# Optimization experiments

Hardware: AMD Instinct MI355X
Metric: run time of the kernel (lower is better)

The kernel has to match this reference:

```python
import jax, jax.numpy as jnp
import numpy as np

D_MODEL = 512
NUM_HEADS = 8
D_HEAD = D_MODEL // NUM_HEADS
B, S = 2, 4096


def setup_inputs() -> dict:
    key = jax.random.key(0)
    ks = jax.random.split(key, 9)
    scale = 1.0 / np.sqrt(D_MODEL)
    x = jax.random.normal(ks[0], (B, S, D_MODEL), dtype=jnp.float32)
    Wq = jax.random.normal(ks[1], (D_MODEL, D_MODEL), dtype=jnp.float32) * scale
    Wk = jax.random.normal(ks[2], (D_MODEL, D_MODEL), dtype=jnp.float32) * scale
    Wv = jax.random.normal(ks[3], (D_MODEL, D_MODEL), dtype=jnp.float32) * scale
    Wo = jax.random.normal(ks[4], (D_MODEL, D_MODEL), dtype=jnp.float32) * scale
    bq = jnp.zeros((D_MODEL,), jnp.float32)
    bk = jnp.zeros((D_MODEL,), jnp.float32)
    bv = jnp.zeros((D_MODEL,), jnp.float32)
    bo = jnp.zeros((D_MODEL,), jnp.float32)
    return {"x": x, "Wq": Wq, "bq": bq, "Wk": Wk, "bk": bk,
            "Wv": Wv, "bv": bv, "Wo": Wo, "bo": bo}


def _split_heads(t):
    # [B, S, D] -> [B, H, S, d_head]
    b, s, _ = t.shape
    return t.reshape(b, s, NUM_HEADS, D_HEAD).transpose(0, 2, 1, 3)


def reference(x, Wq, bq, Wk, bk, Wv, bv, Wo, bo):
    q = _split_heads(x @ Wq + bq)  # [B,H,S,dh]
    k = _split_heads(x @ Wk + bk)
    v = _split_heads(x @ Wv + bv)
    scores = jnp.einsum("bhqd,bhkd->bhqk", q, k) / jnp.sqrt(
        jnp.asarray(D_HEAD, x.dtype))
    attn = jax.nn.softmax(scores, axis=-1)  # dropout is identity at inference
    out = jnp.einsum("bhqk,bhkd->bhqd", attn, v)  # [B,H,S,dh]
    out = out.transpose(0, 2, 1, 3).reshape(x.shape[0], x.shape[1], D_MODEL)
    return out @ Wo + bo
```

## Files before the change

kernel.cpp:

```cpp
#include <hip/hip_runtime.h>
#include <cstddef>

#define NB   2
#define SEQ  4096
#define DM   512
#define NH   8
#define DH   64
#define MTOT 8192
#define KSPLIT 2
#define KSEQ (SEQ / KSPLIT)

#define QSCALE 0.18033688011112042f

typedef __attribute__((ext_vector_type(8))) short short8;
typedef __attribute__((ext_vector_type(4))) float f32x4;

__device__ __forceinline__ ushort f2bf(float f) {
  unsigned u = __builtin_bit_cast(unsigned, f);
  u += 0x7FFFu + ((u >> 16) & 1u);
  return (ushort)(u >> 16);
}
__device__ __forceinline__ float bf2f(ushort b) {
  return __builtin_bit_cast(float, ((unsigned)b) << 16);
}
__device__ __forceinline__ unsigned cvt_pk_bf16(float lo, float hi) {
  unsigned r;
  asm("v_cvt_pk_bf16_f32 %0, %1, %2" : "=v"(r) : "v"(lo), "v"(hi));
  return r;
}
__device__ __forceinline__ float fexp2(float x) {
#if __has_builtin(__builtin_amdgcn_exp2f)
  return __builtin_amdgcn_exp2f(x);
#else
  float r;
  asm("v_exp_f32 %0, %1" : "=v"(r) : "v"(x));
  return r;
#endif
}

__global__ __launch_bounds__(256)
void xcast_k(const float* __restrict__ x, ushort* __restrict__ xb) {
  const int i = (blockIdx.x * 256 + threadIdx.x) * 8;
  float4 a = *(const float4*)(x + i);
  float4 b = *(const float4*)(x + i + 4);
  ushort h[8] = {f2bf(a.x), f2bf(a.y), f2bf(a.z), f2bf(a.w),
                 f2bf(b.x), f2bf(b.y), f2bf(b.z), f2bf(b.w)};
  *(uint4*)(xb + i) = *(const uint4*)h;
}

__global__ __launch_bounds__(256)
void prep_w_k(const float* __restrict__ W, ushort* __restrict__ WT,
              ushort* __restrict__ WTl) {
  __shared__ float t[32][33];
  const int k0 = blockIdx.x * 32, n0 = blockIdx.y * 32;
  const int tx = threadIdx.x & 31, ty = threadIdx.x >> 5;
#pragma unroll
  for (int i = 0; i < 32; i += 8)
    t[ty + i][tx] = W[(size_t)(k0 + ty + i) * DM + n0 + tx];
  __syncthreads();
#pragma unroll
  for (int i = 0; i < 32; i += 8) {
    float v = t[tx][ty + i];
    ushort h = f2bf(v);
    WT[(size_t)(n0 + ty + i) * DM + k0 + tx] = h;
    if (WTl) WTl[(size_t)(n0 + ty + i) * DM + k0 + tx] = f2bf(v - bf2f(h));
  }
}

__global__ __launch_bounds__(256)
void qkv_gemm_k(const ushort* __restrict__ xb,
                const ushort* __restrict__ WTq, const ushort* __restrict__ WTk,
                const ushort* __restrict__ WTv,
                const float* __restrict__ bq, const float* __restrict__ bk,
                const float* __restrict__ bv,
                ushort* __restrict__ Qb, ushort* __restrict__ Kb,
                ushort* __restrict__ Vb) {
  __shared__ ushort smem[64 * 136];
  ushort (*As)[40] = (ushort(*)[40])smem;
  ushort (*Bs)[40] = (ushort(*)[40])(smem + 5120);

  const int z = blockIdx.z;
  const ushort* WT = (z == 0) ? WTq : (z == 1) ? WTk : WTv;
  const float* bias = (z == 0) ? bq : (z == 1) ? bk : bv;
  ushort* outp = (z == 0) ? Qb : (z == 1) ? Kb : Vb;
  const float oscale = (z == 0) ? QSCALE : 1.0f;

  const int tid = threadIdx.x;
  const int w = tid >> 6, l = tid & 63;
  const int g = l >> 4, l15 = l & 15;
  const int wm = w >> 1, wn = w & 1;
  const int m0 = blockIdx.x * 128;
  const int n0 = blockIdx.y * 64;

  const int ar = tid >> 1, ac = (tid & 1) * 16;
  const int br = tid >> 2, bc = (tid & 3) * 8;

  const ushort* Ag = xb + (size_t)(m0 + ar) * DM + ac;
  const ushort* Bg = WT + (size_t)(n0 + br) * DM + bc;

  uint4 ra0 = *(const uint4*)(Ag);
  uint4 ra1 = *(const uint4*)(Ag + 8);
  uint4 rb0 = *(const uint4*)(Bg);

  float bfn[2];
#pragma unroll
  for (int fn = 0; fn < 2; ++fn)
    bfn[fn] = bias[n0 + wn * 32 + fn * 16 + l15];

  f32x4 acc[4][2];
#pragma unroll
  for (int fm = 0; fm < 4; ++fm)
#pragma unroll
    for (int fn = 0; fn < 2; ++fn) acc[fm][fn] = (f32x4){0.f, 0.f, 0.f, 0.f};

  for (int k0 = 0; k0 < DM; k0 += 32) {
    __syncthreads();
    *(uint4*)&As[ar][ac] = ra0;
    *(uint4*)&As[ar][ac + 8] = ra1;
    *(uint4*)&Bs[br][bc] = rb0;
    __syncthreads();
    if (k0 + 32 < DM) {
      ra0 = *(const uint4*)(Ag + k0 + 32);
      ra1 = *(const uint4*)(Ag + k0 + 40);
      rb0 = *(const uint4*)(Bg + k0 + 32);
    }
    short8 af[4], bf[2];
#pragma unroll
    for (int fm = 0; fm < 4; ++fm)
      af[fm] = *(const short8*)&As[wm * 64 + fm * 16 + l15][g * 8];
#pragma unroll
    for (int fn = 0; fn < 2; ++fn)
      bf[fn] = *(const short8*)&Bs[wn * 32 + fn * 16 + l15][g * 8];
#pragma unroll
    for (int fm = 0; fm < 4; ++fm)
#pragma unroll
      for (int fn = 0; fn < 2; ++fn)
        acc[fm][fn] = __builtin_amdgcn_mfma_f32_16x16x32_bf16(
            af[fm], bf[fn], acc[fm][fn], 0, 0, 0);
  }

  if (z != 2) {
#pragma unroll
    for (int fm = 0; fm < 4; ++fm)
#pragma unroll
      for (int fn = 0; fn < 2; ++fn)
#pragma unroll
        for (int r = 0; r < 4; ++r) {
          int m = m0 + wm * 64 + fm * 16 + g * 4 + r;
          int n = n0 + wn * 32 + fn * 16 + l15;
          float v = (acc[fm][fn][r] + bfn[fn]) * oscale;
          int b = m >> 12, s = m & (SEQ - 1);
          int h = n >> 6, d = n & 63;
          outp[(size_t)((b * NH + h) * SEQ + s) * DH + d] = f2bf(v);
        }
  } else {
    __syncthreads();
    ushort (*T)[136] = (ushort(*)[136])smem;
#pragma unroll
    for (int fm = 0; fm < 4; ++fm)
#pragma unroll
      for (int fn = 0; fn < 2; ++fn)
#pragma unroll
        for (int r = 0; r < 4; ++r) {
          int ml = wm * 64 + fm * 16 + g * 4 + r;
          int nl = wn * 32 + fn * 16 + l15;
          T[nl][ml] = f2bf(acc[fm][fn][r] + bfn[fn]);
        }
    __syncthreads();
    const int b = m0 >> 12, h = n0 >> 6, s0 = m0 & (SEQ - 1);
#pragma unroll
    for (int it = 0; it < 4; ++it) {
      int ch = tid + 256 * it;
      int row = ch >> 4;
      int cc = (ch & 15) * 8;
      *(uint4*)&outp[((size_t)(b * NH + h) * DH + row) * SEQ + s0 + cc] =
          *(const uint4*)&T[row][cc];
    }
  }
}

__global__ __launch_bounds__(256)
void oproj_gemm_k(const float* __restrict__ Po, const float* __restrict__ Dn,
                  const ushort* __restrict__ WTh, const ushort* __restrict__ WTl,
                  const float* __restrict__ bo, float* __restrict__ out) {
  __shared__ ushort Ah[128][40];
  __shared__ ushort Al[128][40];
  __shared__ ushort Bh[64][40];
  __shared__ ushort Bl[64][40];

  const int tid = threadIdx.x;
  const int w = tid >> 6, l = tid & 63;
  const int g = l >> 4, l15 = l & 15;
  const int wm = w >> 1, wn = w & 1;
  const int m0 = blockIdx.x * 128;
  const int n0 = blockIdx.y * 64;

  const int ar = tid >> 1, ac = (tid & 1) * 16;
  const int br = tid >> 2, bc = (tid & 3) * 8;

  const int m  = m0 + ar;
  const int bb = m >> 12, ss = m & (SEQ - 1);
  const size_t zoff = (size_t)(NB * NH) * SEQ * DH;

  const ushort* Bhg = WTh + (size_t)(n0 + br) * DM + bc;
  const ushort* Blg = WTl + (size_t)(n0 + br) * DM + bc;

  auto loadA = [&](int c, float* av) {
    const int h = c >> 6, d = c & 63;
    const int bh = bb * NH + h;
    const size_t i0 = ((size_t)bh * SEQ + ss) * DH + d;
    const float den = Dn[(size_t)bh * SEQ + ss] +
                      Dn[(size_t)(NB * NH + bh) * SEQ + ss];
    const float inv = __builtin_amdgcn_rcpf(den);
#pragma unroll
    for (int i = 0; i < 16; i += 4) {
      float4 p0 = *(const float4*)(Po + i0 + i);
      float4 p1 = *(const float4*)(Po + zoff + i0 + i);
      av[i + 0] = (p0.x + p1.x) * inv;
      av[i + 1] = (p0.y + p1.y) * inv;
      av[i + 2] = (p0.z + p1.z) * inv;
      av[i + 3] = (p0.w + p1.w) * inv;
    }
  };

  float av[16];
  loadA(ac, av);
  uint4 rbh = *(const uint4*)Bhg;
  uint4 rbl = *(const uint4*)Blg;

  float bfn[2];
#pragma unroll
  for (int fn = 0; fn < 2; ++fn)
    bfn[fn] = bo[n0 + wn * 32 + fn * 16 + l15];

  f32x4 acc[4][2];
#pragma unroll
  for (int fm = 0; fm < 4; ++fm)
#pragma unroll
    for (int fn = 0; fn < 2; ++fn) acc[fm][fn] = (f32x4){0.f, 0.f, 0.f, 0.f};

  for (int k0 = 0; k0 < DM; k0 += 32) {
    __syncthreads();
    {
      ushort hh[16], ll[16];
#pragma unroll
      for (int i = 0; i < 16; ++i) {
        ushort h = f2bf(av[i]);
        hh[i] = h;
        ll[i] = f2bf(av[i] - bf2f(h));
      }
      *(uint4*)&Ah[ar][ac]     = *(const uint4*)&hh[0];
      *(uint4*)&Ah[ar][ac + 8] = *(const uint4*)&hh[8];
      *(uint4*)&Al[ar][ac]     = *(const uint4*)&ll[0];
      *(uint4*)&Al[ar][ac + 8] = *(const uint4*)&ll[8];
      *(uint4*)&Bh[br][bc] = rbh;
      *(uint4*)&Bl[br][bc] = rbl;
    }
    __syncthreads();
    if (k0 + 32 < DM) {
      loadA(ac + k0 + 32, av);
      rbh = *(const uint4*)(Bhg + k0 + 32);
      rbl = *(const uint4*)(Blg + k0 + 32);
    }
    short8 ah[4], al[4], bh[2], bl[2];
#pragma unroll
    for (int fm = 0; fm < 4; ++fm) {
      ah[fm] = *(const short8*)&Ah[wm * 64 + fm * 16 + l15][g * 8];
      al[fm] = *(const short8*)&Al[wm * 64 + fm * 16 + l15][g * 8];
    }
#pragma unroll
    for (int fn = 0; fn < 2; ++fn) {
      bh[fn] = *(const short8*)&Bh[wn * 32 + fn * 16 + l15][g * 8];
      bl[fn] = *(const short8*)&Bl[wn * 32 + fn * 16 + l15][g * 8];
    }
#pragma unroll
    for (int fm = 0; fm < 4; ++fm)
#pragma unroll
      for (int fn = 0; fn < 2; ++fn) {
        f32x4 c = acc[fm][fn];
        c = __builtin_amdgcn_mfma_f32_16x16x32_bf16(ah[fm], bh[fn], c, 0, 0, 0);
        c = __builtin_amdgcn_mfma_f32_16x16x32_bf16(ah[fm], bl[fn], c, 0, 0, 0);
        c = __builtin_amdgcn_mfma_f32_16x16x32_bf16(al[fm], bh[fn], c, 0, 0, 0);
        acc[fm][fn] = c;
      }
  }

#pragma unroll
  for (int fm = 0; fm < 4; ++fm)
#pragma unroll
    for (int fn = 0; fn < 2; ++fn)
#pragma unroll
      for (int r = 0; r < 4; ++r) {
        int mm = m0 + wm * 64 + fm * 16 + g * 4 + r;
        int n = n0 + wn * 32 + fn * 16 + l15;
        out[(size_t)mm * DM + n] = acc[fm][fn][r] + bfn[fn];
      }
}

__global__ __launch_bounds__(256, 4)
void attn_mfma_k(const ushort* __restrict__ Q, const ushort* __restrict__ K,
                 const ushort* __restrict__ VT, float* __restrict__ Po,
                 float* __restrict__ Dn) {
  __shared__ ushort Ks[2][64][72];
  __shared__ unsigned Vt[2][64][36];

  const int tid = threadIdx.x;
  const int w   = tid >> 6;
  const int l   = tid & 63;
  const int g   = l >> 4;
  const int l15 = l & 15;
  const int bh  = blockIdx.y;
  const int z   = blockIdx.z;
  const int q0  = blockIdx.x * 128 + w * 32;
  const int tb  = z * KSEQ;

  short8 qb[2][2];
#pragma unroll
  for (int qh = 0; qh < 2; ++qh) {
    const ushort* Qrow = Q + ((size_t)bh * SEQ + q0 + qh * 16 + l15) * DH;
    qb[qh][0] = *(const short8*)(Qrow + g * 8);
    qb[qh][1] = *(const short8*)(Qrow + 32 + g * 8);
  }

  short8 vones;
#pragma unroll
  for (int i = 0; i < 8; ++i) vones[i] = (short)0x3F80;

  f32x4 acc[2][4];
  f32x4 accl[2];
#pragma unroll
  for (int qh = 0; qh < 2; ++qh) {
    accl[qh] = (f32x4){0.f, 0.f, 0.f, 0.f};
#pragma unroll
    for (int dt = 0; dt < 4; ++dt) acc[qh][dt] = (f32x4){0.f, 0.f, 0.f, 0.f};
  }

  const ushort* Kg = K + (size_t)bh * SEQ * DH;

  const int rho  = tid >> 2;
  const int kcol = (tid & 3) * 16;
  const int sig  = 32 * ((rho >> 5) & 1) + 8 * ((rho >> 2) & 3) +
                   4 * ((rho >> 4) & 1) + (rho & 3);
  const ushort* Kp = Kg + (size_t)(tb + sig) * DH + kcol;

  const int vrow = tid >> 2;
  const int vcb  = (tid & 3) * 8;
  const unsigned* Vrow =
      (const unsigned*)(VT + ((size_t)bh * DH + vrow) * SEQ) + tb / 2 + vcb;

  uint4 kr0 = *(const uint4*)(Kp);
  uint4 kr1 = *(const uint4*)(Kp + 8);
  uint4 vv0 = *(const uint4*)(Vrow);
  uint4 vv1 = *(const uint4*)(Vrow + 4);

  int cur = 0;
  for (int t0 = 0; t0 < KSEQ; t0 += 64) {
    *(uint4*)&Ks[cur][rho][kcol]     = kr0;
    *(uint4*)&Ks[cur][rho][kcol + 8] = kr1;
    *(uint4*)&Vt[cur][vrow][vcb]     = vv0;
    *(uint4*)&Vt[cur][vrow][vcb + 4] = vv1;
    if (t0 + 64 < KSEQ) {
      kr0 = *(const uint4*)(Kp + (size_t)(t0 + 64) * DH);
      kr1 = *(const uint4*)(Kp + (size_t)(t0 + 64) * DH + 8);
      vv0 = *(const uint4*)(Vrow + (t0 + 64) / 2);
      vv1 = *(const uint4*)(Vrow + (t0 + 64) / 2 + 4);
    }
    __syncthreads();

    f32x4 s[2][4];
    __builtin_amdgcn_s_setprio(1);
#pragma unroll
    for (int nf = 0; nf < 4; ++nf) {
      short8 ka0 = *(const short8*)&Ks[cur][nf * 16 + l15][g * 8];
      short8 ka1 = *(const short8*)&Ks[cur][nf * 16 + l15][32 + g * 8];
#pragma unroll
      for (int qh = 0; qh < 2; ++qh) {
        f32x4 c = (f32x4){0.f, 0.f, 0.f, 0.f};
        c = __builtin_amdgcn_mfma_f32_16x16x32_bf16(ka0, qb[qh][0], c, 0, 0, 0);
        c = __builtin_amdgcn_mfma_f32_16x16x32_bf16(ka1, qb[qh][1], c, 0, 0, 0);
        s[qh][nf] = c;
      }
    }
    __builtin_amdgcn_s_setprio(0);

    short8 pa[2][2];
#pragma unroll
    for (int qh = 0; qh < 2; ++qh) {
      float p[4][4];
#pragma unroll
      for (int nf = 0; nf < 4; ++nf)
#pragma unroll
        for (int r = 0; r < 4; ++r) p[nf][r] = fexp2(s[qh][nf][r]);
      uint4 u0, u1;
      u0.x = cvt_pk_bf16(p[0][0], p[0][1]);
      u0.y = cvt_pk_bf16(p[0][2], p[0][3]);
      u0.z = cvt_pk_bf16(p[1][0], p[1][1]);
      u0.w = cvt_pk_bf16(p[1][2], p[1][3]);
      u1.x = cvt_pk_bf16(p[2][0], p[2][1]);
      u1.y = cvt_pk_bf16(p[2][2], p[2][3]);
      u1.z = cvt_pk_bf16(p[3][0], p[3][1]);
      u1.w = cvt_pk_bf16(p[3][2], p[3][3]);
      pa[qh][0] = __builtin_bit_cast(short8, u0);
      pa[qh][1] = __builtin_bit_cast(short8, u1);
    }

    __builtin_amdgcn_s_setprio(1);
#pragma unroll
    for (int dt = 0; dt < 4; ++dt) {
      short8 vb0 = *(const short8*)&Vt[cur][dt * 16 + l15][4 * g];
      short8 vb1 = *(const short8*)&Vt[cur][dt * 16 + l15][16 + 4 * g];
#pragma unroll
      for (int qh = 0; qh < 2; ++qh) {
        acc[qh][dt] = __builtin_amdgcn_mfma_f32_16x16x32_bf16(pa[qh][0], vb0,
                                                              acc[qh][dt], 0, 0, 0);
        acc[qh][dt] = __builtin_amdgcn_mfma_f32_16x16x32_bf16(pa[qh][1], vb1,
                                                              acc[qh][dt], 0, 0, 0);
      }
    }
#pragma unroll
    for (int qh = 0; qh < 2; ++qh) {
      accl[qh] = __builtin_amdgcn_mfma_f32_16x16x32_bf16(pa[qh][0], vones,
                                                         accl[qh], 0, 0, 0);
      accl[qh] = __builtin_amdgcn_mfma_f32_16x16x32_bf16(pa[qh][1], vones,
                                                         accl[qh], 0, 0, 0);
    }
    __builtin_amdgcn_s_setprio(0);
    cur ^= 1;
  }

  const int zo = z * (NB * NH) + bh;
#pragma unroll
  for (int qh = 0; qh < 2; ++qh) {
#pragma unroll
    for (int dt = 0; dt < 4; ++dt)
#pragma unroll
      for (int r = 0; r < 4; ++r) {
        int srow = q0 + qh * 16 + g * 4 + r;
        Po[((size_t)zo * SEQ + srow) * DH + dt * 16 + l15] = acc[qh][dt][r];
      }
    if (l15 == 0)
#pragma unroll
      for (int r = 0; r < 4; ++r)
        Dn[(size_t)zo * SEQ + q0 + qh * 16 + g * 4 + r] = accl[qh][r];
  }
}

extern "C" void kernel_launch(void* const* d_in, const int* in_sizes, int n_in,
                              void* d_out, int out_size, void* d_ws, size_t ws_size,
                              hipStream_t stream) {
  const float* x  = (const float*)d_in[0];
  const float* Wq = (const float*)d_in[1];
  const float* bq = (const float*)d_in[2];
  const float* Wk = (const float*)d_in[3];
  const float* bk = (const float*)d_in[4];
  const float* Wv = (const float*)d_in[5];
  const float* bv = (const float*)d_in[6];
  const float* Wo = (const float*)d_in[7];
  const float* bo = (const float*)d_in[8];
  float* out = (float*)d_out;

  const size_t per = (size_t)NB * NH * SEQ * DH;
  const size_t wsz = (size_t)DM * DM;
  ushort* xb  = (ushort*)d_ws;
  ushort* WTq = xb + (size_t)MTOT * DM;
  ushort* WTk = WTq + wsz;
  ushort* WTv = WTk + wsz;
  ushort* WTh = WTv + wsz;
  ushort* WTl = WTh + wsz;
  ushort* Qb  = WTl + wsz;
  ushort* Kb  = Qb + per;
  ushort* Vb  = Kb + per;
  float*  Po  = (float*)(Vb + per);
  float*  Dn  = Po + (size_t)KSPLIT * per;

  xcast_k<<<MTOT * DM / (256 * 8), 256, 0, stream>>>(x, xb);
  prep_w_k<<<dim3(16, 16), 256, 0, stream>>>(Wq, WTq, nullptr);
  prep_w_k<<<dim3(16, 16), 256, 0, stream>>>(Wk, WTk, nullptr);
  prep_w_k<<<dim3(16, 16), 256, 0, stream>>>(Wv, WTv, nullptr);
  prep_w_k<<<dim3(16, 16), 256, 0, stream>>>(Wo, WTh, WTl);
  qkv_gemm_k<<<dim3(MTOT / 128, DM / 64, 3), 256, 0, stream>>>(
      xb, WTq, WTk, WTv, bq, bk, bv, Qb, Kb, Vb);
  attn_mfma_k<<<dim3(SEQ / 128, NB * NH, KSPLIT), 256, 0, stream>>>(
      Qb, Kb, Vb, Po, Dn);
  oproj_gemm_k<<<dim3(MTOT / 128, DM / 64), 256, 0, stream>>>(
      Po, Dn, WTh, WTl, bo, out);
}
```

Before: 147.8 us.

## Fuse x bf16 cast into QKV GEMM, widen N tile, batch weight prep

Drops the separate x-to-bf16 cast kernel: the QKV GEMM now loads fp32 x directly and converts it while staging into shared memory. The GEMM N tile is widened from 64 to 128 columns so each block reuses its A tile across more outputs, and the V transpose epilogue now spans two heads. The four weight-prep launches are merged into one launch using a z grid dimension. This removes launches and an intermediate bf16 buffer round trip, at the cost of more accumulator registers, double the A global-load bytes, and half as many GEMM blocks.

```diff
diff --git a/kernel.cpp b/kernel.cpp
--- a/kernel.cpp
+++ b/kernel.cpp
@@ -39,18 +39,16 @@
 }
 
 __global__ __launch_bounds__(256)
-void xcast_k(const float* __restrict__ x, ushort* __restrict__ xb) {
-  const int i = (blockIdx.x * 256 + threadIdx.x) * 8;
-  float4 a = *(const float4*)(x + i);
-  float4 b = *(const float4*)(x + i + 4);
-  ushort h[8] = {f2bf(a.x), f2bf(a.y), f2bf(a.z), f2bf(a.w),
-                 f2bf(b.x), f2bf(b.y), f2bf(b.z), f2bf(b.w)};
-  *(uint4*)(xb + i) = *(const uint4*)h;
-}
-
-__global__ __launch_bounds__(256)
-void prep_w_k(const float* __restrict__ W, ushort* __restrict__ WT,
+void prep_w_k(const float* __restrict__ Wq, const float* __restrict__ Wk,
+              const float* __restrict__ Wv, const float* __restrict__ Wo,
+              ushort* __restrict__ WTq, ushort* __restrict__ WTk,
+              ushort* __restrict__ WTv, ushort* __restrict__ WTh,
               ushort* __restrict__ WTl) {
+  const int z = blockIdx.z;
+  const float* W = (z == 0) ? Wq : (z == 1) ? Wk : (z == 2) ? Wv : Wo;
+  ushort* WT = (z == 0) ? WTq : (z == 1) ? WTk : (z == 2) ? WTv : WTh;
+  ushort* WTlo = (z == 3) ? WTl : nullptr;
+
   __shared__ float t[32][33];
   const int k0 = blockIdx.x * 32, n0 = blockIdx.y * 32;
   const int tx = threadIdx.x & 31, ty = threadIdx.x >> 5;
@@ -63,19 +61,19 @@
     float v = t[tx][ty + i];
     ushort h = f2bf(v);
     WT[(size_t)(n0 + ty + i) * DM + k0 + tx] = h;
-    if (WTl) WTl[(size_t)(n0 + ty + i) * DM + k0 + tx] = f2bf(v - bf2f(h));
+    if (WTlo) WTlo[(size_t)(n0 + ty + i) * DM + k0 + tx] = f2bf(v - bf2f(h));
   }
 }
 
 __global__ __launch_bounds__(256)
-void qkv_gemm_k(const ushort* __restrict__ xb,
+void qkv_gemm_k(const float* __restrict__ x,
                 const ushort* __restrict__ WTq, const ushort* __restrict__ WTk,
                 const ushort* __restrict__ WTv,
                 const float* __restrict__ bq, const float* __restrict__ bk,
                 const float* __restrict__ bv,
                 ushort* __restrict__ Qb, ushort* __restrict__ Kb,
                 ushort* __restrict__ Vb) {
-  __shared__ ushort smem[64 * 136];
+  __shared__ ushort smem[17408];
   ushort (*As)[40] = (ushort(*)[40])smem;
   ushort (*Bs)[40] = (ushort(*)[40])(smem + 5120);
 
@@ -90,51 +88,60 @@
   const int g = l >> 4, l15 = l & 15;
   const int wm = w >> 1, wn = w & 1;
   const int m0 = blockIdx.x * 128;
-  const int n0 = blockIdx.y * 64;
+  const int n0 = blockIdx.y * 128;
 
   const int ar = tid >> 1, ac = (tid & 1) * 16;
-  const int br = tid >> 2, bc = (tid & 3) * 8;
-
-  const ushort* Ag = xb + (size_t)(m0 + ar) * DM + ac;
-  const ushort* Bg = WT + (size_t)(n0 + br) * DM + bc;
-
-  uint4 ra0 = *(const uint4*)(Ag);
-  uint4 ra1 = *(const uint4*)(Ag + 8);
+  const float*  Ag = x  + (size_t)(m0 + ar) * DM + ac;
+  const ushort* Bg = WT + (size_t)(n0 + ar) * DM + ac;
+
+  float av[16];
+#pragma unroll
+  for (int i = 0; i < 16; i += 4)
+    *(float4*)&av[i] = *(const float4*)(Ag + i);
   uint4 rb0 = *(const uint4*)(Bg);
-
-  float bfn[2];
-#pragma unroll
-  for (int fn = 0; fn < 2; ++fn)
-    bfn[fn] = bias[n0 + wn * 32 + fn * 16 + l15];
-
-  f32x4 acc[4][2];
+  uint4 rb1 = *(const uint4*)(Bg + 8);
+
+  float bfn[4];
+#pragma unroll
+  for (int fn = 0; fn < 4; ++fn)
+    bfn[fn] = bias[n0 + wn * 64 + fn * 16 + l15];
+
+  f32x4 acc[4][4];
 #pragma unroll
   for (int fm = 0; fm < 4; ++fm)
 #pragma unroll
-    for (int fn = 0; fn < 2; ++fn) acc[fm][fn] = (f32x4){0.f, 0.f, 0.f, 0.f};
+    for (int fn = 0; fn < 4; ++fn) acc[fm][fn] = (f32x4){0.f, 0.f, 0.f, 0.f};
 
   for (int k0 = 0; k0 < DM; k0 += 32) {
     __syncthreads();
-    *(uint4*)&As[ar][ac] = ra0;
-    *(uint4*)&As[ar][ac + 8] = ra1;
-    *(uint4*)&Bs[br][bc] = rb0;
+    {
+      ushort hh[16];
+#pragma unroll
+      for (int i = 0; i < 16; ++i) hh[i] = f2bf(av[i]);
+      *(uint4*)&As[ar][ac]     = *(const uint4*)&hh[0];
+      *(uint4*)&As[ar][ac + 8] = *(const uint4*)&hh[8];
+      *(uint4*)&Bs[ar][ac]     = rb0;
+      *(uint4*)&Bs[ar][ac + 8] = rb1;
+    }
     __syncthreads();
     if (k0 + 32 < DM) {
-      ra0 = *(const uint4*)(Ag + k0 + 32);
-      ra1 = *(const uint4*)(Ag + k0 + 40);
+#pragma unroll
+      for (int i = 0; i < 16; i += 4)
+        *(float4*)&av[i] = *(const float4*)(Ag + k0 + 32 + i);
       rb0 = *(const uint4*)(Bg + k0 + 32);
-    }
-    short8 af[4], bf[2];
+      rb1 = *(const uint4*)(Bg + k0 + 40);
+    }
+    short8 af[4], bf[4];
 #pragma unroll
     for (int fm = 0; fm < 4; ++fm)
       af[fm] = *(const short8*)&As[wm * 64 + fm * 16 + l15][g * 8];
 #pragma unroll
-    for (int fn = 0; fn < 2; ++fn)
-      bf[fn] = *(const short8*)&Bs[wn * 32 + fn * 16 + l15][g * 8];
+    for (int fn = 0; fn < 4; ++fn)
+      bf[fn] = *(const short8*)&Bs[wn * 64 + fn * 16 + l15][g * 8];
 #pragma unroll
     for (int fm = 0; fm < 4; ++fm)
 #pragma unroll
-      for (int fn = 0; fn < 2; ++fn)
+      for (int fn = 0; fn < 4; ++fn)
         acc[fm][fn] = __builtin_amdgcn_mfma_f32_16x16x32_bf16(
             af[fm], bf[fn], acc[fm][fn], 0, 0, 0);
   }
@@ -143,11 +150,11 @@
 #pragma unroll
     for (int fm = 0; fm < 4; ++fm)
 #pragma unroll
-      for (int fn = 0; fn < 2; ++fn)
+      for (int fn = 0; fn < 4; ++fn)
 #pragma unroll
         for (int r = 0; r < 4; ++r) {
           int m = m0 + wm * 64 + fm * 16 + g * 4 + r;
-          int n = n0 + wn * 32 + fn * 16 + l15;
+          int n = n0 + wn * 64 + fn * 16 + l15;
           float v = (acc[fm][fn][r] + bfn[fn]) * oscale;
           int b = m >> 12, s = m & (SEQ - 1);
           int h = n >> 6, d = n & 63;
@@ -159,21 +166,23 @@
 #pragma unroll
     for (int fm = 0; fm < 4; ++fm)
 #pragma unroll
-      for (int fn = 0; fn < 2; ++fn)
+      for (int fn = 0; fn < 4; ++fn)
 #pragma unroll
         for (int r = 0; r < 4; ++r) {
           int ml = wm * 64 + fm * 16 + g * 4 + r;
-          int nl = wn * 32 + fn * 16 + l15;
+          int nl = wn * 64 + fn * 16 + l15;
           T[nl][ml] = f2bf(acc[fm][fn][r] + bfn[fn]);
         }
     __syncthreads();
-    const int b = m0 >> 12, h = n0 >> 6, s0 = m0 & (SEQ - 1);
-#pragma unroll
-    for (int it = 0; it < 4; ++it) {
+    const int b = m0 >> 12, s0 = m0 & (SEQ - 1);
+#pragma unroll
+    for (int it = 0; it < 8; ++it) {
       int ch = tid + 256 * it;
       int row = ch >> 4;
       int cc = (ch & 15) * 8;
-      *(uint4*)&outp[((size_t)(b * NH + h) * DH + row) * SEQ + s0 + cc] =
+      int n = n0 + row;
+      int h = n >> 6, d = n & 63;
+      *(uint4*)&outp[((size_t)(b * NH + h) * DH + d) * SEQ + s0 + cc] =
           *(const uint4*)&T[row][cc];
     }
   }
@@ -461,8 +470,7 @@
 
   const size_t per = (size_t)NB * NH * SEQ * DH;
   const size_t wsz = (size_t)DM * DM;
-  ushort* xb  = (ushort*)d_ws;
-  ushort* WTq = xb + (size_t)MTOT * DM;
+  ushort* WTq = (ushort*)d_ws;
   ushort* WTk = WTq + wsz;
   ushort* WTv = WTk + wsz;
   ushort* WTh = WTv + wsz;
@@ -473,13 +481,10 @@
   float*  Po  = (float*)(Vb + per);
   float*  Dn  = Po + (size_t)KSPLIT * per;
 
-  xcast_k<<<MTOT * DM / (256 * 8), 256, 0, stream>>>(x, xb);
-  prep_w_k<<<dim3(16, 16), 256, 0, stream>>>(Wq, WTq, nullptr);
-  prep_w_k<<<dim3(16, 16), 256, 0, stream>>>(Wk, WTk, nullptr);
-  prep_w_k<<<dim3(16, 16), 256, 0, stream>>>(Wv, WTv, nullptr);
-  prep_w_k<<<dim3(16, 16), 256, 0, stream>>>(Wo, WTh, WTl);
-  qkv_gemm_k<<<dim3(MTOT / 128, DM / 64, 3), 256, 0, stream>>>(
-      xb, WTq, WTk, WTv, bq, bk, bv, Qb, Kb, Vb);
+  prep_w_k<<<dim3(16, 16, 4), 256, 0, stream>>>(Wq, Wk, Wv, Wo,
+                                                WTq, WTk, WTv, WTh, WTl);
+  qkv_gemm_k<<<dim3(MTOT / 128, DM / 128, 3), 256, 0, stream>>>(
+      x, WTq, WTk, WTv, bq, bk, bv, Qb, Kb, Vb);
   attn_mfma_k<<<dim3(SEQ / 128, NB * NH, KSPLIT), 256, 0, stream>>>(
       Qb, Kb, Vb, Po, Dn);
   oproj_gemm_k<<<dim3(MTOT / 128, DM / 64), 256, 0, stream>>>(
```

Result: no change. 145.1 us (-1.9%).
